# Kernel optimization log

Hardware: AMD Instinct MI355X
Metric: run time of the kernel (lower is better)

## Reference

```python
import jax, jax.numpy as jnp
import numpy as np

SEQ_LEN, IN_DIM = 120, 132
UNITS = (64, 128, 64)
N_LABELS = 101


def _lstm(x, W, U, b):
    """Keras-style LSTM with activation='relu', recurrent_activation='sigmoid'.
    x: (B,T,D), W: (D,4u), U: (u,4u), b: (4u,). Gate order i,f,c,o.
    Returns full hidden sequence (B,T,u)."""
    u = U.shape[0]
    # precompute input projections for all timesteps (big GEMM outside scan)
    xz = jnp.einsum('btd,dz->btz', x, W) + b  # (B,T,4u)

    def step(carry, z_t):
        h, c = carry
        z = z_t + h @ U  # (B,4u)
        i, f, g, o = jnp.split(z, 4, axis=-1)
        i = jax.nn.sigmoid(i)
        f = jax.nn.sigmoid(f)
        o = jax.nn.sigmoid(o)
        c = f * c + i * jax.nn.relu(g)
        h = o * jax.nn.relu(c)
        return (h, c), h

    B = x.shape[0]
    h0 = jnp.zeros((B, u), x.dtype)
    (_, _), hs = jax.lax.scan(step, (h0, h0), jnp.swapaxes(xz, 0, 1))
    return jnp.swapaxes(hs, 0, 1)  # (B,T,u)


def setup_inputs() -> dict:
    key = jax.random.key(0)
    ks = jax.random.split(key, 16)
    s = 0.05
    d = {'x': jax.random.normal(ks[0], (1024, SEQ_LEN, IN_DIM), jnp.float32)}
    in_dims = (IN_DIM,) + UNITS[:-1]
    for l, (din, u) in enumerate(zip(in_dims, UNITS), start=1):
        d[f'W{l}'] = jax.random.normal(ks[3 * l - 2], (din, 4 * u), jnp.float32) * s
        d[f'U{l}'] = jax.random.normal(ks[3 * l - 1], (u, 4 * u), jnp.float32) * s
        d[f'b{l}'] = jnp.zeros((4 * u,), jnp.float32)
    dense_dims = [(UNITS[-1], 64), (64, 32), (32, N_LABELS)]
    for l, (din, dout) in enumerate(dense_dims, start=1):
        d[f'Wd{l}'] = jax.random.normal(ks[9 + l], (din, dout), jnp.float32) * s
        d[f'bd{l}'] = jnp.zeros((dout,), jnp.float32)
    return d


def reference(x, W1, U1, b1, W2, U2, b2, W3, U3, b3,
              Wd1, bd1, Wd2, bd2, Wd3, bd3):
    h = _lstm(x, W1, U1, b1)          # (B,T,64)
    h = _lstm(h, W2, U2, b2)          # (B,T,128)
    h = _lstm(h, W3, U3, b3)[:, -1]   # return_sequences=False -> (B,64)
    h = jax.nn.relu(h @ Wd1 + bd1)    # (B,64)
    h = jax.nn.relu(h @ Wd2 + bd2)    # (B,32)
    return jax.nn.softmax(h @ Wd3 + bd3, axis=-1)  # (B,101)
```

## Files before the change

kernel.cpp:

```cpp
#include <hip/hip_runtime.h>
#include <math.h>

#define T_STEPS 120
#define BATCH   1024

typedef __attribute__((ext_vector_type(8))) short bf16x8;
typedef __attribute__((ext_vector_type(4))) float f32x4;
typedef unsigned short u16;

__device__ __forceinline__ unsigned split2(float f) {
    union { float f; unsigned u; } a; a.f = f;
    unsigned hi = a.u >> 16;
    union { float f; unsigned u; } h; h.u = a.u & 0xFFFF0000u;
    union { float f; unsigned u; } b; b.f = f - h.f;
    unsigned rr = b.u + 0x7FFFu + ((b.u >> 16) & 1);
    return (hi << 16) | (rr >> 16);
}

__device__ __forceinline__ short bf16rne(float f) {
    union { float f; unsigned u; } a; a.f = f;
    unsigned r = a.u + 0x7FFFu + ((a.u >> 16) & 1);
    return (short)(r >> 16);
}

__device__ __forceinline__ float fast_sigmoid(float x) {
    float e = __expf(-x);
    return __builtin_amdgcn_rcpf(1.f + e);
}

__device__ __forceinline__ void block_sync_lds() {
    asm volatile("s_waitcnt lgkmcnt(0)" ::: "memory");
    __builtin_amdgcn_sched_barrier(0);
    __builtin_amdgcn_s_barrier();
    __builtin_amdgcn_sched_barrier(0);
}

__global__ __launch_bounds__(256)
void xconv(const float* __restrict__ x, u16* __restrict__ xhi)
{
    int idx = blockIdx.x * 256 + threadIdx.x;
    int k   = idx % 144;
    int bt  = idx / 144;
    float f = (k < 132) ? x[(size_t)bt * 132 + k] : 0.f;
    xhi[idx] = (u16)(unsigned short)bf16rne(f);
}

template<int U, int NBT, int KXD, int KTX, int KTAIL, bool LAST_ONLY>
__global__ __launch_bounds__(512, 1)
void lstm_comb(const u16* __restrict__ xhi,
               const float* __restrict__ W, int KIN,
               const float* __restrict__ Uw, const float* __restrict__ bias,
               u16* __restrict__ hhi, float* __restrict__ hlast)
{
    constexpr int NZ  = 4 * U;
    constexpr int KTH = U / 32;
    constexpr int KXP = KTX * 32;
    constexpr int HPLANE = NBT * U;
    constexpr int UG  = U / 16;
    static_assert(UG * (NBT / 16) == 8, "8 waves");

    __shared__ u16 hsh[4 * HPLANE];
    __shared__ u16 Wl[KXP * NZ];

    const int tid  = threadIdx.x;
    const int lane = tid & 63;
    const int wid  = tid >> 6;
    const int ln   = lane & 15;
    const int lq   = lane >> 4;
    const int ug   = wid % UG;
    const int bh   = wid / UG;
    const int unit = ug * 16 + ln;
    const int bb   = bh * 16;
    const int b0   = blockIdx.x * NBT;

    for (int idx = tid; idx < KXP * NZ; idx += 512) {
        int k = idx / NZ, n = idx % NZ;
        float f = (k < KIN) ? W[(size_t)k * NZ + n] : 0.f;
        Wl[((k >> 3) * NZ + n) * 8 + (k & 7)] = (u16)bf16rne(f);
    }

    bf16x8 bwu[4][KTH];
#pragma unroll
    for (int p = 0; p < 4; ++p)
#pragma unroll
        for (int kt = 0; kt < KTH; ++kt)
#pragma unroll
            for (int e = 0; e < 8; ++e) {
                int k = kt * 32 + lq * 8 + e;
                bwu[p][kt][e] = bf16rne(Uw[(size_t)k * NZ + p * U + unit]);
            }
    float breg[4];
#pragma unroll
    for (int p = 0; p < 4; ++p) breg[p] = bias[p * U + unit];

    u16* hw0 = hsh + ((unit >> 3) * NBT + bb + lq * 4) * 8 + (unit & 7);
    u16* hw1 = hw0 + 2 * HPLANE;
    float creg[4];
#pragma unroll
    for (int r = 0; r < 4; ++r) {
        creg[r] = 0.f;
        hw0[r * 8] = 0;
        hw0[HPLANE + r * 8] = 0;
    }

    const u16* hrd[2][KTH];
#pragma unroll
    for (int b = 0; b < 2; ++b)
#pragma unroll
        for (int kt = 0; kt < KTH; ++kt)
            hrd[b][kt] = hsh + b * 2 * HPLANE + ((kt * 4 + lq) * NBT + bb + ln) * 8;

    const u16* wb = Wl + ((size_t)lq * NZ + unit) * 8;

    const u16* pxh = xhi + ((size_t)(b0 + bb + ln) * T_STEPS) * KXD + lq * 8;
    bf16x8 xfh[KTX] = {};
#pragma unroll
    for (int kt = 0; kt < KTX; ++kt)
        if (kt < KTX - 1 || lq < KTAIL)
            xfh[kt] = *reinterpret_cast<const bf16x8*>(pxh + kt * 32);

    size_t ho = ((size_t)(b0 + bb + lq * 4) * T_STEPS) * U + unit;

    block_sync_lds();

#define CSTEP(CUR, OTH, tc)                                                     \
    {                                                                           \
        f32x4 acc[4] = {};                                                      \
        _Pragma("unroll")                                                       \
        for (int kt = 0; kt < KTH; ++kt) {                                      \
            bf16x8 ahh = *reinterpret_cast<const bf16x8*>(hrd[CUR][kt]);        \
            bf16x8 ahl = *reinterpret_cast<const bf16x8*>(hrd[CUR][kt] + HPLANE); \
            _Pragma("unroll")                                                   \
            for (int p = 0; p < 4; ++p) {                                       \
                acc[p] = __builtin_amdgcn_mfma_f32_16x16x32_bf16(ahh, bwu[p][kt], acc[p], 0, 0, 0); \
                acc[p] = __builtin_amdgcn_mfma_f32_16x16x32_bf16(ahl, bwu[p][kt], acc[p], 0, 0, 0); \
            }                                                                   \
        }                                                                       \
        _Pragma("unroll")                                                       \
        for (int kt = 0; kt < KTX; ++kt)                                        \
        _Pragma("unroll")                                                       \
        for (int p = 0; p < 4; ++p) {                                           \
            bf16x8 wf = *reinterpret_cast<const bf16x8*>(wb + ((size_t)kt * 4 * NZ + p * U) * 8); \
            acc[p] = __builtin_amdgcn_mfma_f32_16x16x32_bf16(xfh[kt], wf, acc[p], 0, 0, 0); \
        }                                                                       \
        if ((tc) + 1 < T_STEPS) {                                               \
            pxh += KXD;                                                         \
            _Pragma("unroll")                                                   \
            for (int kt = 0; kt < KTX; ++kt)                                    \
                if (kt < KTX - 1 || lq < KTAIL)                                 \
                    xfh[kt] = *reinterpret_cast<const bf16x8*>(pxh + kt * 32);  \
        }                                                                       \
        _Pragma("unroll")                                                       \
        for (int r = 0; r < 4; ++r) {                                           \
            float si = fast_sigmoid(acc[0][r] + breg[0]);                       \
            float sf = fast_sigmoid(acc[1][r] + breg[1]);                       \
            float gg = fmaxf(acc[2][r] + breg[2], 0.f);                         \
            float so = fast_sigmoid(acc[3][r] + breg[3]);                       \
            float c  = sf * creg[r] + si * gg;                                  \
            creg[r] = c;                                                        \
            float h = so * fmaxf(c, 0.f);                                       \
            unsigned s = split2(h);                                             \
            u16* hw = (OTH) ? hw1 : hw0;                                        \
            hw[r * 8] = (u16)(s >> 16);                                         \
            hw[HPLANE + r * 8] = (u16)s;                                        \
            if constexpr (!LAST_ONLY) {                                         \
                hhi[ho + (size_t)r * (T_STEPS * U) + (size_t)(tc) * U] = (u16)(s >> 16); \
            } else {                                                            \
                if ((tc) == T_STEPS - 1)                                        \
                    hlast[(size_t)(b0 + bb + lq * 4 + r) * U + unit] = h;       \
            }                                                                   \
        }                                                                       \
        block_sync_lds();                                                       \
    }

    for (int t = 0; t < T_STEPS; t += 2) {
        CSTEP(0, 1, t)
        CSTEP(1, 0, t + 1)
    }
#undef CSTEP
}

__global__ __launch_bounds__(256)
void dense_head(const float* __restrict__ h3,
                const float* __restrict__ Wd1, const float* __restrict__ bd1,
                const float* __restrict__ Wd2, const float* __restrict__ bd2,
                const float* __restrict__ Wd3, const float* __restrict__ bd3,
                float* __restrict__ out)
{
    __shared__ float s1[4][64];
    __shared__ float s2[4][32];
    const int w    = threadIdx.x >> 6;
    const int lane = threadIdx.x & 63;
    const int row  = blockIdx.x * 4 + w;

    float hval = h3[(size_t)row * 64 + lane];
    float a = bd1[lane];
#pragma unroll
    for (int k = 0; k < 64; ++k) {
        float hk = __shfl(hval, k, 64);
        a = fmaf(hk, Wd1[k * 64 + lane], a);
    }
    s1[w][lane] = fmaxf(a, 0.f);
    __syncthreads();

    if (lane < 32) {
        float a2 = bd2[lane];
#pragma unroll
        for (int k = 0; k < 64; ++k) a2 = fmaf(s1[w][k], Wd2[k * 32 + lane], a2);
        s2[w][lane] = fmaxf(a2, 0.f);
    }
    __syncthreads();

    float a0 = bd3[lane];
#pragma unroll
    for (int k = 0; k < 32; ++k) a0 = fmaf(s2[w][k], Wd3[k * 101 + lane], a0);
    float a1 = -INFINITY;
    if (lane < 37) {
        a1 = bd3[64 + lane];
#pragma unroll
        for (int k = 0; k < 32; ++k) a1 = fmaf(s2[w][k], Wd3[k * 101 + 64 + lane], a1);
    }

    float m = fmaxf(a0, a1);
#pragma unroll
    for (int off = 32; off > 0; off >>= 1) m = fmaxf(m, __shfl_xor(m, off, 64));
    float e0 = expf(a0 - m);
    float e1 = (lane < 37) ? expf(a1 - m) : 0.f;
    float s = e0 + e1;
#pragma unroll
    for (int off = 32; off > 0; off >>= 1) s += __shfl_xor(s, off, 64);

    out[(size_t)row * 101 + lane] = e0 / s;
    if (lane < 37) out[(size_t)row * 101 + 64 + lane] = e1 / s;
}

extern "C" void kernel_launch(void* const* d_in, const int* in_sizes, int n_in,
                              void* d_out, int out_size, void* d_ws, size_t ws_size,
                              hipStream_t stream) {
    const float* x   = (const float*)d_in[0];
    const float* W1  = (const float*)d_in[1];
    const float* U1  = (const float*)d_in[2];
    const float* b1  = (const float*)d_in[3];
    const float* W2  = (const float*)d_in[4];
    const float* U2  = (const float*)d_in[5];
    const float* b2  = (const float*)d_in[6];
    const float* W3  = (const float*)d_in[7];
    const float* U3  = (const float*)d_in[8];
    const float* b3  = (const float*)d_in[9];
    const float* Wd1 = (const float*)d_in[10];
    const float* bd1 = (const float*)d_in[11];
    const float* Wd2 = (const float*)d_in[12];
    const float* bd2 = (const float*)d_in[13];
    const float* Wd3 = (const float*)d_in[14];
    const float* bd3 = (const float*)d_in[15];

    u16* ws16 = (u16*)d_ws;
    u16* xhi  = ws16;
    u16* h2hi = ws16;
    u16* h1hi = ws16 + 17694720;
    float* h3 = (float*)(ws16 + 25559040);

    xconv<<<(BATCH * T_STEPS * 144) / 256, 256, 0, stream>>>(x, xhi);
    lstm_comb<64, 32, 144, 5, 2, false><<<32, 512, 0, stream>>>(
        xhi, W1, 132, U1, b1, h1hi, nullptr);
    lstm_comb<128, 16, 64, 2, 4, false><<<64, 512, 0, stream>>>(
        h1hi, W2, 64, U2, b2, h2hi, nullptr);
    lstm_comb<64, 32, 128, 4, 4, true><<<32, 512, 0, stream>>>(
        h2hi, W3, 128, U3, b3, nullptr, h3);
    dense_head<<<BATCH / 4, 256, 0, stream>>>(h3, Wd1, bd1, Wd2, bd2, Wd3, bd3,
                                              (float*)d_out);
}
```

Baseline: 529.7 us.

## Store LSTM inputs and hidden sequences in MFMA fragment-ready time-major layout

Converts x and the intermediate hidden sequences into a fragment-tiled, time-major layout indexed by [t][batch-block][k-tile][lane][8]. Each wave's per-step x loads then become fully contiguous 16-byte lane reads, replacing strided per-batch rows. The tail predicates go away because padding is baked into the layout. Writes of h become scattered 2-byte stores into fragment positions, and the workspace no longer aliases buffers, so it uses more memory.

Measured after the change: 495.8 us. 1.07x faster.

```diff
diff --git a/kernel.cpp b/kernel.cpp
--- a/kernel.cpp
+++ b/kernel.cpp
@@ -3,9 +3,11 @@
 
 #define T_STEPS 120
 #define BATCH   1024
+#define NBK     64
 
 typedef __attribute__((ext_vector_type(8))) short bf16x8;
 typedef __attribute__((ext_vector_type(4))) float f32x4;
+typedef __attribute__((ext_vector_type(4))) unsigned short us4;
 typedef unsigned short u16;
 
 __device__ __forceinline__ unsigned split2(float f) {
@@ -36,27 +38,46 @@
 }
 
 __global__ __launch_bounds__(256)
-void xconv(const float* __restrict__ x, u16* __restrict__ xhi)
+void xconv(const float* __restrict__ x, u16* __restrict__ xf)
 {
-    int idx = blockIdx.x * 256 + threadIdx.x;
-    int k   = idx % 144;
-    int bt  = idx / 144;
-    float f = (k < 132) ? x[(size_t)bt * 132 + k] : 0.f;
-    xhi[idx] = (u16)(unsigned short)bf16rne(f);
-}
-
-template<int U, int NBT, int KXD, int KTX, int KTAIL, bool LAST_ONLY>
+    int tid  = blockIdx.x * 256 + threadIdx.x;
+    int lane = tid & 63;
+    int rest = tid >> 6;
+    int kt   = rest % 5;
+    int tbk  = rest / 5;
+    int bk   = tbk & 63;
+    int t    = tbk >> 6;
+    int ln   = lane & 15, lq = lane >> 4;
+    int b    = bk * 16 + ln;
+    int k0   = kt * 32 + lq * 8;
+    const float* src = &x[((size_t)b * T_STEPS + t) * 132];
+    u16 out[8];
+#pragma unroll
+    for (int e = 0; e < 8; ++e) {
+        int k = k0 + e;
+        out[e] = (u16)bf16rne((k < 132) ? src[k] : 0.f);
+    }
+    us4 o0, o1;
+    o0.x = out[0]; o0.y = out[1]; o0.z = out[2]; o0.w = out[3];
+    o1.x = out[4]; o1.y = out[5]; o1.z = out[6]; o1.w = out[7];
+    *reinterpret_cast<us4*>(&xf[(size_t)tid * 8])     = o0;
+    *reinterpret_cast<us4*>(&xf[(size_t)tid * 8 + 4]) = o1;
+}
+
+template<int U, int NBT, int KTXI, int KTXO, bool LAST_ONLY>
 __global__ __launch_bounds__(512, 1)
-void lstm_comb(const u16* __restrict__ xhi,
+void lstm_comb(const u16* __restrict__ xf,
                const float* __restrict__ W, int KIN,
                const float* __restrict__ Uw, const float* __restrict__ bias,
-               u16* __restrict__ hhi, float* __restrict__ hlast)
+               u16* __restrict__ hf, float* __restrict__ hlast)
 {
     constexpr int NZ  = 4 * U;
     constexpr int KTH = U / 32;
-    constexpr int KXP = KTX * 32;
+    constexpr int KXP = KTXI * 32;
     constexpr int HPLANE = NBT * U;
     constexpr int UG  = U / 16;
+    constexpr size_t XSTRIDE = (size_t)NBK * KTXI * 512;
+    constexpr size_t OSTRIDE = (size_t)NBK * KTXO * 512;
     static_assert(UG * (NBT / 16) == 8, "8 waves");
 
     __shared__ u16 hsh[4 * HPLANE];
@@ -72,6 +93,7 @@
     const int unit = ug * 16 + ln;
     const int bb   = bh * 16;
     const int b0   = blockIdx.x * NBT;
+    const int bkw  = (b0 + bb) >> 4;
 
     for (int idx = tid; idx < KXP * NZ; idx += 512) {
         int k = idx / NZ, n = idx % NZ;
@@ -112,14 +134,19 @@
 
     const u16* wb = Wl + ((size_t)lq * NZ + unit) * 8;
 
-    const u16* pxh = xhi + ((size_t)(b0 + bb + ln) * T_STEPS) * KXD + lq * 8;
-    bf16x8 xfh[KTX] = {};
-#pragma unroll
-    for (int kt = 0; kt < KTX; ++kt)
-        if (kt < KTX - 1 || lq < KTAIL)
-            xfh[kt] = *reinterpret_cast<const bf16x8*>(pxh + kt * 32);
-
-    size_t ho = ((size_t)(b0 + bb + lq * 4) * T_STEPS) * U + unit;
+    const u16* pxf = xf + ((size_t)bkw * KTXI) * 512 + lane * 8;
+    bf16x8 xfh[KTXI];
+#pragma unroll
+    for (int kt = 0; kt < KTXI; ++kt)
+        xfh[kt] = *reinterpret_cast<const bf16x8*>(pxf + kt * 512);
+
+    u16* hfo = nullptr;
+    if constexpr (!LAST_ONLY) {
+        int kto = unit >> 5;
+        int lqp = (unit >> 3) & 3;
+        int ep  = unit & 7;
+        hfo = hf + (((size_t)bkw * KTXO + kto) * 64 + lqp * 16 + lq * 4) * 8 + ep;
+    }
 
     block_sync_lds();
 
@@ -137,18 +164,17 @@
             }                                                                   \
         }                                                                       \
         _Pragma("unroll")                                                       \
-        for (int kt = 0; kt < KTX; ++kt)                                        \
+        for (int kt = 0; kt < KTXI; ++kt)                                       \
         _Pragma("unroll")                                                       \
         for (int p = 0; p < 4; ++p) {                                           \
             bf16x8 wf = *reinterpret_cast<const bf16x8*>(wb + ((size_t)kt * 4 * NZ + p * U) * 8); \
             acc[p] = __builtin_amdgcn_mfma_f32_16x16x32_bf16(xfh[kt], wf, acc[p], 0, 0, 0); \
         }                                                                       \
         if ((tc) + 1 < T_STEPS) {                                               \
-            pxh += KXD;                                                         \
+            pxf += XSTRIDE;                                                     \
             _Pragma("unroll")                                                   \
-            for (int kt = 0; kt < KTX; ++kt)                                    \
-                if (kt < KTX - 1 || lq < KTAIL)                                 \
-                    xfh[kt] = *reinterpret_cast<const bf16x8*>(pxh + kt * 32);  \
+            for (int kt = 0; kt < KTXI; ++kt)                                   \
+                xfh[kt] = *reinterpret_cast<const bf16x8*>(pxf + kt * 512);     \
         }                                                                       \
         _Pragma("unroll")                                                       \
         for (int r = 0; r < 4; ++r) {                                           \
@@ -164,7 +190,7 @@
             hw[r * 8] = (u16)(s >> 16);                                         \
             hw[HPLANE + r * 8] = (u16)s;                                        \
             if constexpr (!LAST_ONLY) {                                         \
-                hhi[ho + (size_t)r * (T_STEPS * U) + (size_t)(tc) * U] = (u16)(s >> 16); \
+                hfo[(size_t)(tc) * OSTRIDE + r * 8] = (u16)(s >> 16);           \
             } else {                                                            \
                 if ((tc) == T_STEPS - 1)                                        \
                     hlast[(size_t)(b0 + bb + lq * 4 + r) * U + unit] = h;       \
@@ -255,18 +281,18 @@
     const float* bd3 = (const float*)d_in[15];
 
     u16* ws16 = (u16*)d_ws;
-    u16* xhi  = ws16;
-    u16* h2hi = ws16;
-    u16* h1hi = ws16 + 17694720;
-    float* h3 = (float*)(ws16 + 25559040);
-
-    xconv<<<(BATCH * T_STEPS * 144) / 256, 256, 0, stream>>>(x, xhi);
-    lstm_comb<64, 32, 144, 5, 2, false><<<32, 512, 0, stream>>>(
-        xhi, W1, 132, U1, b1, h1hi, nullptr);
-    lstm_comb<128, 16, 64, 2, 4, false><<<64, 512, 0, stream>>>(
-        h1hi, W2, 64, U2, b2, h2hi, nullptr);
-    lstm_comb<64, 32, 128, 4, 4, true><<<32, 512, 0, stream>>>(
-        h2hi, W3, 128, U3, b3, nullptr, h3);
+    u16* xfb  = ws16;
+    u16* h1f  = ws16 + 19660800;
+    u16* h2f  = h1f + 7864320;
+    float* h3 = (float*)(ws16 + 43253760);
+
+    xconv<<<(T_STEPS * NBK * 5 * 64) / 256, 256, 0, stream>>>(x, xfb);
+    lstm_comb<64, 32, 5, 2, false><<<32, 512, 0, stream>>>(
+        xfb, W1, 132, U1, b1, h1f, nullptr);
+    lstm_comb<128, 16, 2, 4, false><<<64, 512, 0, stream>>>(
+        h1f, W2, 64, U2, b2, h2f, nullptr);
+    lstm_comb<64, 32, 4, 1, true><<<32, 512, 0, stream>>>(
+        h2f, W3, 128, U3, b3, nullptr, h3);
     dense_head<<<BATCH / 4, 256, 0, stream>>>(h3, Wd1, bd1, Wd2, bd2, Wd3, bd3,
                                               (float*)d_out);
 }
```
